# Performance work log

Hardware: AMD Instinct MI355X
Metric: run time of the kernel (lower is better)

Reference implementation:

```python
import jax, jax.numpy as jnp
import numpy as np

N_NODES = 30000
N_EDGES = 480000
F_IN = 64
F_EDGE = 16
HID = 128
N_LAYERS = 3
N_CLASSES = 10
MSG_EPS = 1e-7   # GENConv eps added after ReLU
SM_EPS = 1e-16   # PyG softmax denom eps
LN_EPS = 1e-5


def _layer_norm(x, g, b):
    m = jnp.mean(x, axis=-1, keepdims=True)
    v = jnp.mean((x - m) ** 2, axis=-1, keepdims=True)
    return (x - m) * jax.lax.rsqrt(v + LN_EPS) * g + b


def _gen_conv(h, ea, src, dst, t, w1, b1, lg, lb, w2, b2):
    # GENConv message: relu(x_j + e_ij) + eps  -> [E, H]
    msg = jax.nn.relu(h[src] + ea) + MSG_EPS
    # learnable-temperature segment softmax over incoming edges of each node
    logits = msg * t
    mx = jax.ops.segment_max(logits, dst, num_segments=N_NODES)
    e = jnp.exp(logits - mx[dst])
    s = jax.ops.segment_sum(e, dst, num_segments=N_NODES)
    alpha = e / (s[dst] + SM_EPS)
    agg = jax.ops.segment_sum(msg * alpha, dst, num_segments=N_NODES)  # [N, H]
    # out = MLP(aggr + x): Linear(H,2H) -> LayerNorm -> ReLU -> Linear(2H,H)
    z = agg + h
    z = jax.nn.relu(_layer_norm(z @ w1 + b1, lg, lb)) @ w2 + b2
    return z


def setup_inputs() -> dict:
    key = jax.random.key(0)
    ks = jax.random.split(key, 10)
    g = lambda k, s, sc=0.05: jax.random.normal(k, s, jnp.float32) * sc
    return {
        "x": g(ks[0], (N_NODES, F_IN), 1.0),
        "edge_attr": g(ks[1], (N_EDGES, F_EDGE), 1.0),
        "node_enc_w": g(ks[2], (F_IN, HID)),
        "node_enc_b": jnp.zeros((HID,), jnp.float32),
        "edge_enc_w": g(ks[3], (F_EDGE, HID)),
        "edge_enc_b": jnp.zeros((HID,), jnp.float32),
        "mlp1_w": g(ks[4], (N_LAYERS, HID, 2 * HID)),
        "mlp1_b": jnp.zeros((N_LAYERS, 2 * HID), jnp.float32),
        "mlp_ln_g": jnp.ones((N_LAYERS, 2 * HID), jnp.float32),
        "mlp_ln_b": jnp.zeros((N_LAYERS, 2 * HID), jnp.float32),
        "mlp2_w": g(ks[5], (N_LAYERS, 2 * HID, HID)),
        "mlp2_b": jnp.zeros((N_LAYERS, HID), jnp.float32),
        "t": jnp.ones((N_LAYERS,), jnp.float32),
        "norm_g": jnp.ones((N_LAYERS, HID), jnp.float32),
        "norm_b": jnp.zeros((N_LAYERS, HID), jnp.float32),
        "lin_w": g(ks[6], (HID, N_CLASSES)),
        "lin_b": jnp.zeros((N_CLASSES,), jnp.float32),
        "edge_index": jax.random.randint(ks[7], (2, N_EDGES), 0, N_NODES, jnp.int32),
    }


def reference(x, edge_attr, node_enc_w, node_enc_b, edge_enc_w, edge_enc_b,
              mlp1_w, mlp1_b, mlp_ln_g, mlp_ln_b, mlp2_w, mlp2_b, t,
              norm_g, norm_b, lin_w, lin_b, edge_index):
    src, dst = edge_index[0], edge_index[1]
    ea = edge_attr @ edge_enc_w + edge_enc_b   # [E, H]
    h = x @ node_enc_w + node_enc_b            # [N, H]
    # first layer applies the conv directly (as in the original forward)
    h = _gen_conv(h, ea, src, dst, t[0], mlp1_w[0], mlp1_b[0],
                  mlp_ln_g[0], mlp_ln_b[0], mlp2_w[0], mlp2_b[0])
    # remaining DeepGCN res+ layers: h = h + conv(dropout(relu(norm(h))))
    for i in range(1, N_LAYERS):
        res = h
        z = jax.nn.relu(_layer_norm(h, norm_g[i], norm_b[i]))  # dropout p=0.1 -> identity in eval
        z = _gen_conv(z, ea, src, dst, t[i], mlp1_w[i], mlp1_b[i],
                      mlp_ln_g[i], mlp_ln_b[i], mlp2_w[i], mlp2_b[i])
        h = z + res
    # final norm/act from layers[0] then classifier (dropout -> identity in eval)
    h = jax.nn.relu(_layer_norm(h, norm_g[0], norm_b[0]))
    return h @ lin_w + lin_b
```

## Files before the change

### kernel.cpp

```cpp
#include <hip/hip_runtime.h>
#include <hip/hip_bf16.h>

#define NN 30000
#define NE 480000
#define NROWT 1875

typedef __attribute__((ext_vector_type(8))) short short8;
typedef __attribute__((ext_vector_type(4))) float floatx4;

__device__ __forceinline__ short f2bs(float f) {
    __hip_bfloat16 h = __float2bfloat16(f);
    return *reinterpret_cast<short*>(&h);
}

__device__ __forceinline__ short2 split_bf16(float f) {
    __hip_bfloat16 h = __float2bfloat16(f);
    float r = f - __bfloat162float(h);
    __hip_bfloat16 l = __float2bfloat16(r);
    short2 out;
    out.x = *reinterpret_cast<short*>(&h);
    out.y = *reinterpret_cast<short*>(&l);
    return out;
}

__global__ void presplit_all(const float* __restrict__ ew, const float* __restrict__ nw,
                             const float* __restrict__ m1w, const float* __restrict__ m2w,
                             const float* __restrict__ lw,
                             short* __restrict__ ew_h, short* __restrict__ ew_l,
                             short* __restrict__ nw_h, short* __restrict__ nw_l,
                             short* __restrict__ m1_h, short* __restrict__ m1_l,
                             short* __restrict__ m2_h, short* __restrict__ m2_l,
                             short* __restrict__ lw_h, short* __restrict__ lw_l)
{
    int i = blockIdx.x * 256 + threadIdx.x;
    if (i < 2048) {
        int k = i >> 7, n = i & 127;
        short2 s = split_bf16(ew[i]);
        ew_h[n * 16 + k] = s.x; ew_l[n * 16 + k] = s.y;
    } else if (i < 10240) {
        int j = i - 2048;
        int k = j >> 7, n = j & 127;
        short2 s = split_bf16(nw[j]);
        nw_h[n * 64 + k] = s.x; nw_l[n * 64 + k] = s.y;
    } else if (i < 108544) {
        int j = i - 10240;
        int l = j >> 15, jj = j & 32767;
        int k = jj >> 8, n = jj & 255;
        short2 s = split_bf16(m1w[j]);
        m1_h[(size_t)l * 32768 + n * 128 + k] = s.x;
        m1_l[(size_t)l * 32768 + n * 128 + k] = s.y;
    } else if (i < 206848) {
        int j = i - 108544;
        int l = j >> 15, jj = j & 32767;
        int k = jj >> 7, n = jj & 127;
        short2 s = split_bf16(m2w[j]);
        m2_h[(size_t)l * 32768 + n * 256 + k] = s.x;
        m2_l[(size_t)l * 32768 + n * 256 + k] = s.y;
    } else if (i < 208896) {
        int j = i - 206848;
        int k = j >> 4, n = j & 15;
        short2 s = (n < 10) ? split_bf16(lw[k * 10 + n]) : short2{0, 0};
        lw_h[n * 128 + k] = s.x; lw_l[n * 128 + k] = s.y;
    }
}

template<int K, int N>
__launch_bounds__(256)
__global__ void gemm_a32(const float* __restrict__ A, const short* __restrict__ Bh,
                         const short* __restrict__ Bl, const float* __restrict__ bias,
                         float* __restrict__ C, unsigned* __restrict__ hp, int total_waves)
{
    int wave = ((blockIdx.x * 256) + threadIdx.x) >> 6;
    if (wave >= total_waves) return;
    constexpr int NT = N / 16;
    const int mt = wave / NT, nt = wave % NT;
    const int lane = threadIdx.x & 63;
    const int l15 = lane & 15, quad = lane >> 4;
    const int row = mt * 16 + l15;
    const int col = nt * 16 + l15;
    floatx4 acc = {0.f, 0.f, 0.f, 0.f};
#pragma unroll
    for (int k0 = 0; k0 < K; k0 += 32) {
        const int kb = k0 + quad * 8;
        short8 ah, al;
        const float* ap = A + (size_t)row * K + kb;
        floatx4 a0 = *(const floatx4*)ap;
        floatx4 a1 = *(const floatx4*)(ap + 4);
#pragma unroll
        for (int j = 0; j < 4; j++) {
            short2 s0 = split_bf16(a0[j]); ah[j] = s0.x; al[j] = s0.y;
            short2 s1 = split_bf16(a1[j]); ah[j + 4] = s1.x; al[j + 4] = s1.y;
        }
        short8 bh = *(const short8*)(Bh + (size_t)col * K + kb);
        short8 bl = *(const short8*)(Bl + (size_t)col * K + kb);
        acc = __builtin_amdgcn_mfma_f32_16x16x32_bf16(ah, bh, acc, 0, 0, 0);
        acc = __builtin_amdgcn_mfma_f32_16x16x32_bf16(al, bh, acc, 0, 0, 0);
        acc = __builtin_amdgcn_mfma_f32_16x16x32_bf16(ah, bl, acc, 0, 0, 0);
    }
    float bv = bias[col];
#pragma unroll
    for (int r = 0; r < 4; r++) {
        int ro = mt * 16 + quad * 4 + r;
        float v = acc[r] + bv;
        C[(size_t)ro * N + col] = v;
        int mb = (int)(unsigned short)f2bs(v);
        int ob = __shfl_xor(mb, 1, 64);
        if ((l15 & 1) == 0)
            hp[(size_t)ro * 64 + nt * 8 + (l15 >> 1)] = (unsigned)mb | ((unsigned)ob << 16);
    }
}

template<int K, int NTOT, int NTW, int NREAL>
__launch_bounds__(256)
__global__ void gemm_s(const short* __restrict__ Ah, const short* __restrict__ Al,
                       const short* __restrict__ Bh, const short* __restrict__ Bl,
                       const float* __restrict__ bias, float* __restrict__ C, int total_waves)
{
    int wave = ((blockIdx.x * 256) + threadIdx.x) >> 6;
    if (wave >= total_waves) return;
    constexpr int NG = NTOT / (16 * NTW);
    const int mt = wave / NG, g = wave % NG;
    const int lane = threadIdx.x & 63;
    const int l15 = lane & 15, quad = lane >> 4;
    const int row = mt * 16 + l15;
    floatx4 acc[NTW];
#pragma unroll
    for (int t = 0; t < NTW; t++) acc[t] = {0.f, 0.f, 0.f, 0.f};
#pragma unroll
    for (int k0 = 0; k0 < K; k0 += 32) {
        const int kb = k0 + quad * 8;
        short8 ah = *(const short8*)(Ah + (size_t)row * K + kb);
        short8 al = *(const short8*)(Al + (size_t)row * K + kb);
#pragma unroll
        for (int t = 0; t < NTW; t++) {
            int col = g * NTW * 16 + t * 16 + l15;
            short8 bh = *(const short8*)(Bh + (size_t)col * K + kb);
            short8 bl = *(const short8*)(Bl + (size_t)col * K + kb);
            acc[t] = __builtin_amdgcn_mfma_f32_16x16x32_bf16(ah, bh, acc[t], 0, 0, 0);
            acc[t] = __builtin_amdgcn_mfma_f32_16x16x32_bf16(al, bh, acc[t], 0, 0, 0);
            acc[t] = __builtin_amdgcn_mfma_f32_16x16x32_bf16(ah, bl, acc[t], 0, 0, 0);
        }
    }
#pragma unroll
    for (int t = 0; t < NTW; t++) {
        int col = g * NTW * 16 + t * 16 + l15;
        if (col < NREAL) {
            float bv = bias[col];
#pragma unroll
            for (int r = 0; r < 4; r++) {
                int ro = mt * 16 + quad * 4 + r;
                C[(size_t)ro * NREAL + col] = acc[t][r] + bv;
            }
        }
    }
}

__launch_bounds__(256)
__global__ void gemm_ea(const float* __restrict__ edge_attr, const int* __restrict__ eidx_csr,
                        const short* __restrict__ Bh, const short* __restrict__ Bl,
                        const float* __restrict__ bias, unsigned* __restrict__ ea4)
{
    __shared__ short tile[2][16][132];
    const int wv = threadIdx.x >> 6;
    const int sub = wv >> 1, g = wv & 1;
    const int lane = threadIdx.x & 63;
    const int l15 = lane & 15, quad = lane >> 4;
    const int p = blockIdx.x * 32 + sub * 16 + l15;
    short8 a;
    if (quad < 2) {
        int e = eidx_csr[p];
        const float* ap = edge_attr + (size_t)e * 16 + quad * 8;
        floatx4 a0 = *(const floatx4*)ap;
        floatx4 a1 = *(const floatx4*)(ap + 4);
#pragma unroll
        for (int j = 0; j < 4; j++) { a[j] = f2bs(a0[j]); a[j + 4] = f2bs(a1[j]); }
    } else {
#pragma unroll
        for (int j = 0; j < 8; j++) a[j] = 0;
    }
    floatx4 acc[4];
#pragma unroll
    for (int t = 0; t < 4; t++) acc[t] = {0.f, 0.f, 0.f, 0.f};
#pragma unroll
    for (int t = 0; t < 4; t++) {
        int col = g * 64 + t * 16 + l15;
        short8 bh, bl;
        if (quad < 2) {
            bh = *(const short8*)(Bh + (size_t)col * 16 + quad * 8);
            bl = *(const short8*)(Bl + (size_t)col * 16 + quad * 8);
        } else {
#pragma unroll
            for (int j = 0; j < 8; j++) { bh[j] = 0; bl[j] = 0; }
        }
        acc[t] = __builtin_amdgcn_mfma_f32_16x16x32_bf16(a, bh, acc[t], 0, 0, 0);
        acc[t] = __builtin_amdgcn_mfma_f32_16x16x32_bf16(a, bl, acc[t], 0, 0, 0);
    }
#pragma unroll
    for (int t = 0; t < 4; t++) {
        int col = g * 64 + t * 16 + l15;
        float bv = bias[col];
#pragma unroll
        for (int r = 0; r < 4; r++)
            tile[sub][quad * 4 + r][col] = f2bs(acc[t][r] + bv);
    }
    __syncthreads();
#pragma unroll
    for (int c = 0; c < 2; c++) {
        int idx = threadIdx.x + 256 * c;
        int o = idx * 16;
        int g4l = o >> 10;
        int lp = (o & 1023) >> 4;
        unsigned u[4];
#pragma unroll
        for (int e = 0; e < 4; e++) {
            int rl = g4l * 4 + e;
            u[e] = *(const unsigned*)&tile[rl >> 4][rl & 15][2 * lp];
        }
        uint4 val = make_uint4(u[0], u[1], u[2], u[3]);
        *(uint4*)((char*)ea4 + (size_t)blockIdx.x * 8192 + o) = val;
    }
}

__global__ void zero_kernel(int* __restrict__ p, int n)
{
    int i = blockIdx.x * 256 + threadIdx.x;
    if (i < n) p[i] = 0;
}

__global__ void hist_kernel(const int* __restrict__ dst, int* __restrict__ count)
{
    int e = blockIdx.x * 256 + threadIdx.x;
    if (e < NE) atomicAdd(count + dst[e], 1);
}

__launch_bounds__(1024)
__global__ void scan_kernel(const int* __restrict__ count, int* __restrict__ rowptr)
{
    __shared__ int part[1024];
    const int t = threadIdx.x;
    const int CH = (NN + 1023) / 1024;
    const int base = t * CH;
    int sum = 0;
    for (int j = 0; j < CH; j++) {
        int idx = base + j;
        if (idx < NN) sum += count[idx];
    }
    part[t] = sum;
    __syncthreads();
    for (int d = 1; d < 1024; d <<= 1) {
        int v = (t >= d) ? part[t - d] : 0;
        __syncthreads();
        part[t] += v;
        __syncthreads();
    }
    int off = (t == 0) ? 0 : part[t - 1];
    for (int j = 0; j < CH; j++) {
        int idx = base + j;
        if (idx < NN) { rowptr[idx] = off; off += count[idx]; }
    }
    if (t == 1023) rowptr[NN] = part[1023];
}

__global__ void scatter_kernel(const int* __restrict__ src, const int* __restrict__ dst,
                               const int* __restrict__ rowptr, int* __restrict__ cursor,
                               int* __restrict__ src_csr, int* __restrict__ eidx_csr)
{
    int e = blockIdx.x * 256 + threadIdx.x;
    if (e >= NE) return;
    int d = dst[e];
    int pos = rowptr[d] + atomicAdd(cursor + d, 1);
    src_csr[pos] = src[e];
    eidx_csr[pos] = e;
}

__device__ __forceinline__ void updm(float hv, float av, float tt, float m,
                                     float& s, float& n)
{
    float g = fmaxf(hv + av, 0.f) + 1e-7f;
    float e = __expf(g * tt) * m;
    s += e;
    n = fmaf(g, e, n);
}

__launch_bounds__(256)
__global__ void agg_kernel(const unsigned* __restrict__ hp, const float* __restrict__ hres,
                           const uint4* __restrict__ ea4q, const int* __restrict__ src_csr,
                           const int* __restrict__ rowptr, const float* __restrict__ tptr,
                           int layer, short* __restrict__ Zh, short* __restrict__ Zl)
{
    int node = (blockIdx.x * 256 + threadIdx.x) >> 6;
    if (node >= NN) return;
    const int lane = threadIdx.x & 63;
    const float tt = tptr[layer];
    const int start = rowptr[node];
    const int end = rowptr[node + 1];
    const int g0 = start >> 2, g1 = (end + 3) >> 2;
    float s0 = 0.f, s1 = 0.f, n0 = 0.f, n1 = 0.f;
    float s0b = 0.f, s1b = 0.f, n0b = 0.f, n1b = 0.f;

#define PROC(GG, S0, S1, N0, N1)                                                   \
    {                                                                              \
        uint4 uu = ea4q[((size_t)(GG) << 6) + lane];                               \
        int4 sv = *(const int4*)(src_csr + 4 * (GG));                              \
        int jb = 4 * (GG);                                                         \
        float m0 = (jb     >= start && jb     < end) ? 1.f : 0.f;                  \
        float m1 = (jb + 1 >= start && jb + 1 < end) ? 1.f : 0.f;                  \
        float m2 = (jb + 2 >= start && jb + 2 < end) ? 1.f : 0.f;                  \
        float m3 = (jb + 3 >= start && jb + 3 < end) ? 1.f : 0.f;                  \
        unsigned ha = hp[(size_t)sv.x * 64 + lane];                                \
        unsigned hb = hp[(size_t)sv.y * 64 + lane];                                \
        unsigned hc = hp[(size_t)sv.z * 64 + lane];                                \
        unsigned hd = hp[(size_t)sv.w * 64 + lane];                                \
        updm(__uint_as_float(ha << 16), __uint_as_float(uu.x << 16), tt, m0, S0, N0); \
        updm(__uint_as_float(ha & 0xffff0000u), __uint_as_float(uu.x & 0xffff0000u), tt, m0, S1, N1); \
        updm(__uint_as_float(hb << 16), __uint_as_float(uu.y << 16), tt, m1, S0, N0); \
        updm(__uint_as_float(hb & 0xffff0000u), __uint_as_float(uu.y & 0xffff0000u), tt, m1, S1, N1); \
        updm(__uint_as_float(hc << 16), __uint_as_float(uu.z << 16), tt, m2, S0, N0); \
        updm(__uint_as_float(hc & 0xffff0000u), __uint_as_float(uu.z & 0xffff0000u), tt, m2, S1, N1); \
        updm(__uint_as_float(hd << 16), __uint_as_float(uu.w << 16), tt, m3, S0, N0); \
        updm(__uint_as_float(hd & 0xffff0000u), __uint_as_float(uu.w & 0xffff0000u), tt, m3, S1, N1); \
    }

    int g = g0;
    for (; g + 2 <= g1; g += 2) {
        PROC(g, s0, s1, n0, n1);
        PROC(g + 1, s0b, s1b, n0b, n1b);
    }
    if (g < g1) PROC(g, s0, s1, n0, n1);
#undef PROC
    s0 += s0b; s1 += s1b; n0 += n0b; n1 += n1b;

    float2 res = ((const float2*)hres)[(size_t)node * 64 + lane];
    float ox = n0 / (s0 + 1e-16f) + res.x;
    float oy = n1 / (s1 + 1e-16f) + res.y;
    short2 sx = split_bf16(ox), sy = split_bf16(oy);
    ((unsigned*)Zh)[(size_t)node * 64 + lane] =
        (unsigned)(unsigned short)sx.x | ((unsigned)(unsigned short)sy.x << 16);
    ((unsigned*)Zl)[(size_t)node * 64 + lane] =
        (unsigned)(unsigned short)sx.y | ((unsigned)(unsigned short)sy.y << 16);
}

template<bool HAS_RES, bool FINAL>
__launch_bounds__(256)
__global__ void mlp_fused(const short* __restrict__ Ah, const short* __restrict__ Al,
                          const short* __restrict__ B1h, const short* __restrict__ B1l,
                          const float* __restrict__ b1, const float* __restrict__ g1,
                          const float* __restrict__ be1,
                          const short* __restrict__ B2h, const short* __restrict__ B2l,
                          const float* __restrict__ b2, const float* __restrict__ res,
                          const float* __restrict__ g2, const float* __restrict__ be2,
                          short* __restrict__ z1h,
                          float* __restrict__ Hout, float* __restrict__ HinOut,
                          unsigned* __restrict__ HP,
                          short* __restrict__ Fh, short* __restrict__ Fl)
{
    __shared__ __align__(16) short lds[32768];
    const int wv = threadIdx.x >> 6;
    const int lane = threadIdx.x & 63;
    const int l15 = lane & 15, quad = lane >> 4;
    const int tile = blockIdx.x * 4 + wv;
    const bool valid = (tile < NROWT);
    const int row = tile * 16 + l15;

    floatx4 acc[16];
#pragma unroll
    for (int t = 0; t < 16; t++) acc[t] = {0.f, 0.f, 0.f, 0.f};
    for (int hf = 0; hf < 2; hf++) {
        __syncthreads();
        {
            const float4* s1p = (const float4*)(B1h + hf * 16384);
            const float4* s2p = (const float4*)(B1l + hf * 16384);
            float4* d = (float4*)lds;
#pragma unroll
            for (int i = 0; i < 8; i++) {
                int t8 = threadIdx.x + 256 * i;
                int col = t8 >> 4, k8 = t8 & 15;
                int unit = col * 16 + (k8 ^ (col & 15));
                d[unit] = s1p[t8];
                d[2048 + unit] = s2p[t8];
            }
        }
        __syncthreads();
        if (valid) {
#pragma unroll
            for (int k0 = 0; k0 < 128; k0 += 32) {
                const int kb = k0 + quad * 8;
                const int kb8 = kb >> 3;
                short8 ah = *(const short8*)(Ah + (size_t)row * 128 + kb);
                short8 al = *(const short8*)(Al + (size_t)row * 128 + kb);
#pragma unroll
                for (int t = 0; t < 8; t++) {
                    int col = t * 16 + l15;
                    int unit = col * 16 + (kb8 ^ (col & 15));
                    const short* bp = lds + unit * 8;
                    short8 bh = *(const short8*)bp;
                    short8 bl = *(const short8*)(bp + 16384);
                    int ti = hf * 8 + t;
                    acc[ti] = __builtin_amdgcn_mfma_f32_16x16x32_bf16(ah, bh, acc[ti], 0, 0, 0);
                    acc[ti] = __builtin_amdgcn_mfma_f32_16x16x32_bf16(al, bh, acc[ti], 0, 0, 0);
                    acc[ti] = __builtin_amdgcn_mfma_f32_16x16x32_bf16(ah, bl, acc[ti], 0, 0, 0);
                }
            }
        }
    }
    if (valid) {
#pragma unroll
        for (int t = 0; t < 16; t++) {
            float bv = b1[t * 16 + l15];
#pragma unroll
            for (int r = 0; r < 4; r++) acc[t][r] += bv;
        }
        float s1[4] = {0.f, 0.f, 0.f, 0.f}, s2[4] = {0.f, 0.f, 0.f, 0.f};
#pragma unroll
        for (int t = 0; t < 16; t++)
#pragma unroll
            for (int r = 0; r < 4; r++) { s1[r] += acc[t][r]; s2[r] += acc[t][r] * acc[t][r]; }
#pragma unroll
        for (int m = 1; m <= 8; m <<= 1)
#pragma unroll
            for (int r = 0; r < 4; r++) {
                s1[r] += __shfl_xor(s1[r], m, 64);
                s2[r] += __shfl_xor(s2[r], m, 64);
            }
        float mean[4], rstd[4];
#pragma unroll
        for (int r = 0; r < 4; r++) {
            mean[r] = s1[r] * (1.f / 256.f);
            float var = s2[r] * (1.f / 256.f) - mean[r] * mean[r];
            rstd[r] = rsqrtf(var + 1e-5f);
        }
#pragma unroll
        for (int t = 0; t < 16; t++) {
            int col = t * 16 + l15;
            float gg = g1[col], bb = be1[col];
#pragma unroll
            for (int r = 0; r < 4; r++) {
                float y = fmaxf((acc[t][r] - mean[r]) * rstd[r] * gg + bb, 0.f);
                int ro = tile * 16 + quad * 4 + r;
                z1h[(size_t)ro * 256 + col] = f2bs(y);
            }
        }
    }
    floatx4 acc2[8];
#pragma unroll
    for (int t = 0; t < 8; t++) acc2[t] = {0.f, 0.f, 0.f, 0.f};
    for (int hf = 0; hf < 2; hf++) {
        __syncthreads();
        {
            const float4* s1p = (const float4*)(B2h + hf * 16384);
            const float4* s2p = (const float4*)(B2l + hf * 16384);
            float4* d = (float4*)lds;
#pragma unroll
            for (int i = 0; i < 8; i++) {
                int t8 = threadIdx.x + 256 * i;
                int col = t8 >> 5, k8 = t8 & 31;
                int unit = col * 32 + (k8 ^ (col & 15));
                d[unit] = s1p[t8];
                d[2048 + unit] = s2p[t8];
            }
        }
        __syncthreads();
        if (valid) {
#pragma unroll
            for (int k0 = 0; k0 < 256; k0 += 32) {
                const int kb = k0 + quad * 8;
                const int kb8 = kb >> 3;
                short8 zh = *(const short8*)(z1h + (size_t)row * 256 + kb);
#pragma unroll
                for (int t = 0; t < 4; t++) {
                    int col = t * 16 + l15;
                    int unit = col * 32 + (kb8 ^ (col & 15));
                    const short* bp = lds + unit * 8;
                    short8 bh = *(const short8*)bp;
                    short8 bl = *(const short8*)(bp + 16384);
                    int ti = hf * 4 + t;
                    acc2[ti] = __builtin_amdgcn_mfma_f32_16x16x32_bf16(zh, bh, acc2[ti], 0, 0, 0);
                    acc2[ti] = __builtin_amdgcn_mfma_f32_16x16x32_bf16(zh, bl, acc2[ti], 0, 0, 0);
                }
            }
        }
    }
    if (valid) {
#pragma unroll
        for (int t = 0; t < 8; t++) {
            int col = t * 16 + l15;
            float bv = b2[col];
#pragma unroll
            for (int r = 0; r < 4; r++) {
                acc2[t][r] += bv;
                if (HAS_RES) {
                    int ro = tile * 16 + quad * 4 + r;
                    acc2[t][r] += res[(size_t)ro * 128 + col];
                }
            }
        }
        float s1[4] = {0.f, 0.f, 0.f, 0.f}, s2[4] = {0.f, 0.f, 0.f, 0.f};
#pragma unroll
        for (int t = 0; t < 8; t++)
#pragma unroll
            for (int r = 0; r < 4; r++) { s1[r] += acc2[t][r]; s2[r] += acc2[t][r] * acc2[t][r]; }
#pragma unroll
        for (int m = 1; m <= 8; m <<= 1)
#pragma unroll
            for (int r = 0; r < 4; r++) {
                s1[r] += __shfl_xor(s1[r], m, 64);
                s2[r] += __shfl_xor(s2[r], m, 64);
            }
        float mean[4], rstd[4];
#pragma unroll
        for (int r = 0; r < 4; r++) {
            mean[r] = s1[r] * (1.f / 128.f);
            float var = s2[r] * (1.f / 128.f) - mean[r] * mean[r];
            rstd[r] = rsqrtf(var + 1e-5f);
        }
#pragma unroll
        for (int t = 0; t < 8; t++) {
            int col = t * 16 + l15;
            float gg = g2[col], bb = be2[col];
#pragma unroll
            for (int r = 0; r < 4; r++) {
                int ro = tile * 16 + quad * 4 + r;
                float x = acc2[t][r];
                float y = fmaxf((x - mean[r]) * rstd[r] * gg + bb, 0.f);
                if (FINAL) {
                    short2 sp = split_bf16(y);
                    Fh[(size_t)ro * 128 + col] = sp.x;
                    Fl[(size_t)ro * 128 + col] = sp.y;
                } else {
                    Hout[(size_t)ro * 128 + col] = x;
                    HinOut[(size_t)ro * 128 + col] = y;
                    int yb = (int)(unsigned short)f2bs(y);
                    int ob = __shfl_xor(yb, 1, 64);
                    if ((l15 & 1) == 0)
                        HP[(size_t)ro * 64 + t * 8 + (l15 >> 1)] =
                            (unsigned)yb | ((unsigned)ob << 16);
                }
            }
        }
    }
}

extern "C" void kernel_launch(void* const* d_in, const int* in_sizes, int n_in,
                              void* d_out, int out_size, void* d_ws, size_t ws_size,
                              hipStream_t stream)
{
    const float* x         = (const float*)d_in[0];
    const float* edge_attr = (const float*)d_in[1];
    const float* nw        = (const float*)d_in[2];
    const float* nb        = (const float*)d_in[3];
    const float* ew        = (const float*)d_in[4];
    const float* eb        = (const float*)d_in[5];
    const float* m1w       = (const float*)d_in[6];
    const float* m1b       = (const float*)d_in[7];
    const float* lng       = (const float*)d_in[8];
    const float* lnb       = (const float*)d_in[9];
    const float* m2w       = (const float*)d_in[10];
    const float* m2b       = (const float*)d_in[11];
    const float* tpr       = (const float*)d_in[12];
    const float* ng        = (const float*)d_in[13];
    const float* nbb       = (const float*)d_in[14];
    const float* lw        = (const float*)d_in[15];
    const float* lb        = (const float*)d_in[16];
    const int* ei  = (const int*)d_in[17];
    const int* src = ei;
    const int* dst = ei + NE;

    char* w = (char*)d_ws;
    unsigned* ea4 = (unsigned*)w; w += (size_t)NE * 128 * 2;
    int* src_csr  = (int*)w; w += (size_t)NE * 4;
    int* eidx_csr = (int*)w; w += (size_t)NE * 4;
    unsigned* hp  = (unsigned*)w; w += (size_t)NN * 64 * 4;
    float* h   = (float*)w; w += (size_t)NN * 128 * 4;
    float* hin = (float*)w; w += (size_t)NN * 128 * 4;
    short* zbuf_h = (short*)w; w += (size_t)NN * 128 * 2;
    short* zbuf_l = (short*)w; w += (size_t)NN * 128 * 2;
    short* fin_h  = (short*)w; w += (size_t)NN * 128 * 2;
    short* fin_l  = (short*)w; w += (size_t)NN * 128 * 2;
    short* z1s_h  = (short*)w; w += (size_t)NN * 256 * 2;
    short* ew_h = (short*)w; w += (size_t)128 * 16 * 2;
    short* ew_l = (short*)w; w += (size_t)128 * 16 * 2;
    short* nw_h = (short*)w; w += (size_t)128 * 64 * 2;
    short* nw_l = (short*)w; w += (size_t)128 * 64 * 2;
    short* m1_h = (short*)w; w += (size_t)3 * 256 * 128 * 2;
    short* m1_l = (short*)w; w += (size_t)3 * 256 * 128 * 2;
    short* m2_h = (short*)w; w += (size_t)3 * 128 * 256 * 2;
    short* m2_l = (short*)w; w += (size_t)3 * 128 * 256 * 2;
    short* lw_h = (short*)w; w += (size_t)16 * 128 * 2;
    short* lw_l = (short*)w; w += (size_t)16 * 128 * 2;
    int* count  = (int*)w;   w += (size_t)NN * 4;
    int* cursor = (int*)w;   w += (size_t)NN * 4;
    int* rowptr = (int*)w;   w += (size_t)(NN + 1) * 4;

    zero_kernel<<<(2 * NN + 255) / 256, 256, 0, stream>>>(count, 2 * NN);
    hist_kernel<<<(NE + 255) / 256, 256, 0, stream>>>(dst, count);
    scan_kernel<<<1, 1024, 0, stream>>>(count, rowptr);
    scatter_kernel<<<(NE + 255) / 256, 256, 0, stream>>>(src, dst, rowptr, cursor,
                                                         src_csr, eidx_csr);

    presplit_all<<<(208896 + 255) / 256, 256, 0, stream>>>(
        ew, nw, m1w, m2w, lw, ew_h, ew_l, nw_h, nw_l, m1_h, m1_l, m2_h, m2_l, lw_h, lw_l);

    gemm_ea<<<NE / 32, 256, 0, stream>>>(edge_attr, eidx_csr, ew_h, ew_l, eb, ea4);
    gemm_a32<64, 128><<<(NN / 16) * 8 / 4, 256, 0, stream>>>(x, nw_h, nw_l, nb, h, hp,
                                                             (NN / 16) * 8);

    const uint4* ea4q = (const uint4*)ea4;
    const int mgrid = (NROWT + 3) / 4;
    for (int layer = 0; layer < 3; ++layer) {
        const float* hi = (layer == 0) ? h : hin;
        agg_kernel<<<NN / 4, 256, 0, stream>>>(hp, hi, ea4q, src_csr, rowptr, tpr, layer,
                                               zbuf_h, zbuf_l);
        if (layer == 0) {
            mlp_fused<false, false><<<mgrid, 256, 0, stream>>>(
                zbuf_h, zbuf_l, m1_h, m1_l, m1b, lng, lnb,
                m2_h, m2_l, m2b, nullptr, ng + 128, nbb + 128,
                z1s_h, h, hin, hp, nullptr, nullptr);
        } else if (layer == 1) {
            mlp_fused<true, false><<<mgrid, 256, 0, stream>>>(
                zbuf_h, zbuf_l, m1_h + 32768, m1_l + 32768, m1b + 256, lng + 256, lnb + 256,
                m2_h + 32768, m2_l + 32768, m2b + 128, h, ng + 256, nbb + 256,
                z1s_h, h, hin, hp, nullptr, nullptr);
        } else {
            mlp_fused<true, true><<<mgrid, 256, 0, stream>>>(
                zbuf_h, zbuf_l, m1_h + 65536, m1_l + 65536, m1b + 512, lng + 512, lnb + 512,
                m2_h + 65536, m2_l + 65536, m2b + 256, h, ng, nbb,
                z1s_h, nullptr, nullptr, nullptr, fin_h, fin_l);
        }
    }
    gemm_s<128, 16, 1, 10><<<((NN / 16) + 3) / 4, 256, 0, stream>>>(
        fin_h, fin_l, lw_h, lw_l, lb, (float*)d_out, NN / 16);
}
```

Baseline: 484.3 us.

## Drop low bf16 split for aggregated input and unroll edge loop four ways

The aggregation kernel now writes one bf16 copy of its output instead of a hi/lo split pair, and the first MLP GEMM drops the matching lo*hi MFMA. This halves that intermediate's write and read traffic and removes a third of the MFMAs in the first GEMM. The edge loop is also unrolled four ways with separate accumulators to expose more memory-level parallelism on the gathers. Accuracy of the MLP input drops to plain bf16, which could exceed tolerance.

```diff
diff --git a/kernel.cpp b/kernel.cpp
--- a/kernel.cpp
+++ b/kernel.cpp
@@ -286,7 +286,7 @@
 __global__ void agg_kernel(const unsigned* __restrict__ hp, const float* __restrict__ hres,
                            const uint4* __restrict__ ea4q, const int* __restrict__ src_csr,
                            const int* __restrict__ rowptr, const float* __restrict__ tptr,
-                           int layer, short* __restrict__ Zh, short* __restrict__ Zl)
+                           int layer, unsigned* __restrict__ Zp)
 {
     int node = (blockIdx.x * 256 + threadIdx.x) >> 6;
     if (node >= NN) return;
@@ -295,10 +295,10 @@
     const int start = rowptr[node];
     const int end = rowptr[node + 1];
     const int g0 = start >> 2, g1 = (end + 3) >> 2;
-    float s0 = 0.f, s1 = 0.f, n0 = 0.f, n1 = 0.f;
-    float s0b = 0.f, s1b = 0.f, n0b = 0.f, n1b = 0.f;
-
-#define PROC(GG, S0, S1, N0, N1)                                                   \
+    float S0[4] = {0.f, 0.f, 0.f, 0.f}, S1[4] = {0.f, 0.f, 0.f, 0.f};
+    float N0[4] = {0.f, 0.f, 0.f, 0.f}, N1[4] = {0.f, 0.f, 0.f, 0.f};
+
+#define PROC(GG, U)                                                                \
     {                                                                              \
         uint4 uu = ea4q[((size_t)(GG) << 6) + lane];                               \
         int4 sv = *(const int4*)(src_csr + 4 * (GG));                              \
@@ -311,38 +311,40 @@
         unsigned hb = hp[(size_t)sv.y * 64 + lane];                                \
         unsigned hc = hp[(size_t)sv.z * 64 + lane];                                \
         unsigned hd = hp[(size_t)sv.w * 64 + lane];                                \
-        updm(__uint_as_float(ha << 16), __uint_as_float(uu.x << 16), tt, m0, S0, N0); \
-        updm(__uint_as_float(ha & 0xffff0000u), __uint_as_float(uu.x & 0xffff0000u), tt, m0, S1, N1); \
-        updm(__uint_as_float(hb << 16), __uint_as_float(uu.y << 16), tt, m1, S0, N0); \
-        updm(__uint_as_float(hb & 0xffff0000u), __uint_as_float(uu.y & 0xffff0000u), tt, m1, S1, N1); \
-        updm(__uint_as_float(hc << 16), __uint_as_float(uu.z << 16), tt, m2, S0, N0); \
-        updm(__uint_as_float(hc & 0xffff0000u), __uint_as_float(uu.z & 0xffff0000u), tt, m2, S1, N1); \
-        updm(__uint_as_float(hd << 16), __uint_as_float(uu.w << 16), tt, m3, S0, N0); \
-        updm(__uint_as_float(hd & 0xffff0000u), __uint_as_float(uu.w & 0xffff0000u), tt, m3, S1, N1); \
+        updm(__uint_as_float(ha << 16), __uint_as_float(uu.x << 16), tt, m0, S0[U], N0[U]); \
+        updm(__uint_as_float(ha & 0xffff0000u), __uint_as_float(uu.x & 0xffff0000u), tt, m0, S1[U], N1[U]); \
+        updm(__uint_as_float(hb << 16), __uint_as_float(uu.y << 16), tt, m1, S0[U], N0[U]); \
+        updm(__uint_as_float(hb & 0xffff0000u), __uint_as_float(uu.y & 0xffff0000u), tt, m1, S1[U], N1[U]); \
+        updm(__uint_as_float(hc << 16), __uint_as_float(uu.z << 16), tt, m2, S0[U], N0[U]); \
+        updm(__uint_as_float(hc & 0xffff0000u), __uint_as_float(uu.z & 0xffff0000u), tt, m2, S1[U], N1[U]); \
+        updm(__uint_as_float(hd << 16), __uint_as_float(uu.w << 16), tt, m3, S0[U], N0[U]); \
+        updm(__uint_as_float(hd & 0xffff0000u), __uint_as_float(uu.w & 0xffff0000u), tt, m3, S1[U], N1[U]); \
     }
 
     int g = g0;
-    for (; g + 2 <= g1; g += 2) {
-        PROC(g, s0, s1, n0, n1);
-        PROC(g + 1, s0b, s1b, n0b, n1b);
-    }
-    if (g < g1) PROC(g, s0, s1, n0, n1);
+    for (; g + 4 <= g1; g += 4) {
+        PROC(g,     0);
+        PROC(g + 1, 1);
+        PROC(g + 2, 2);
+        PROC(g + 3, 3);
+    }
+    for (; g < g1; g++) PROC(g, 0);
 #undef PROC
-    s0 += s0b; s1 += s1b; n0 += n0b; n1 += n1b;
+    float s0 = (S0[0] + S0[1]) + (S0[2] + S0[3]);
+    float s1 = (S1[0] + S1[1]) + (S1[2] + S1[3]);
+    float n0 = (N0[0] + N0[1]) + (N0[2] + N0[3]);
+    float n1 = (N1[0] + N1[1]) + (N1[2] + N1[3]);
 
     float2 res = ((const float2*)hres)[(size_t)node * 64 + lane];
     float ox = n0 / (s0 + 1e-16f) + res.x;
     float oy = n1 / (s1 + 1e-16f) + res.y;
-    short2 sx = split_bf16(ox), sy = split_bf16(oy);
-    ((unsigned*)Zh)[(size_t)node * 64 + lane] =
-        (unsigned)(unsigned short)sx.x | ((unsigned)(unsigned short)sy.x << 16);
-    ((unsigned*)Zl)[(size_t)node * 64 + lane] =
-        (unsigned)(unsigned short)sx.y | ((unsigned)(unsigned short)sy.y << 16);
+    Zp[(size_t)node * 64 + lane] =
+        (unsigned)(unsigned short)f2bs(ox) | ((unsigned)(unsigned short)f2bs(oy) << 16);
 }
 
 template<bool HAS_RES, bool FINAL>
 __launch_bounds__(256)
-__global__ void mlp_fused(const short* __restrict__ Ah, const short* __restrict__ Al,
+__global__ void mlp_fused(const short* __restrict__ Ap,
                           const short* __restrict__ B1h, const short* __restrict__ B1l,
                           const float* __restrict__ b1, const float* __restrict__ g1,
                           const float* __restrict__ be1,
@@ -386,8 +388,7 @@
             for (int k0 = 0; k0 < 128; k0 += 32) {
                 const int kb = k0 + quad * 8;
                 const int kb8 = kb >> 3;
-                short8 ah = *(const short8*)(Ah + (size_t)row * 128 + kb);
-                short8 al = *(const short8*)(Al + (size_t)row * 128 + kb);
+                short8 ah = *(const short8*)(Ap + (size_t)row * 128 + kb);
 #pragma unroll
                 for (int t = 0; t < 8; t++) {
                     int col = t * 16 + l15;
@@ -397,7 +398,6 @@
                     short8 bl = *(const short8*)(bp + 16384);
                     int ti = hf * 8 + t;
                     acc[ti] = __builtin_amdgcn_mfma_f32_16x16x32_bf16(ah, bh, acc[ti], 0, 0, 0);
-                    acc[ti] = __builtin_amdgcn_mfma_f32_16x16x32_bf16(al, bh, acc[ti], 0, 0, 0);
                     acc[ti] = __builtin_amdgcn_mfma_f32_16x16x32_bf16(ah, bl, acc[ti], 0, 0, 0);
                 }
             }
@@ -570,10 +570,9 @@
     int* src_csr  = (int*)w; w += (size_t)NE * 4;
     int* eidx_csr = (int*)w; w += (size_t)NE * 4;
     unsigned* hp  = (unsigned*)w; w += (size_t)NN * 64 * 4;
+    unsigned* zp  = (unsigned*)w; w += (size_t)NN * 64 * 4;
     float* h   = (float*)w; w += (size_t)NN * 128 * 4;
     float* hin = (float*)w; w += (size_t)NN * 128 * 4;
-    short* zbuf_h = (short*)w; w += (size_t)NN * 128 * 2;
-    short* zbuf_l = (short*)w; w += (size_t)NN * 128 * 2;
     short* fin_h  = (short*)w; w += (size_t)NN * 128 * 2;
     short* fin_l  = (short*)w; w += (size_t)NN * 128 * 2;
     short* z1s_h  = (short*)w; w += (size_t)NN * 256 * 2;
@@ -608,21 +607,20 @@
     const int mgrid = (NROWT + 3) / 4;
     for (int layer = 0; layer < 3; ++layer) {
         const float* hi = (layer == 0) ? h : hin;
-        agg_kernel<<<NN / 4, 256, 0, stream>>>(hp, hi, ea4q, src_csr, rowptr, tpr, layer,
-                                               zbuf_h, zbuf_l);
+        agg_kernel<<<NN / 4, 256, 0, stream>>>(hp, hi, ea4q, src_csr, rowptr, tpr, layer, zp);
         if (layer == 0) {
             mlp_fused<false, false><<<mgrid, 256, 0, stream>>>(
-                zbuf_h, zbuf_l, m1_h, m1_l, m1b, lng, lnb,
+                (const short*)zp, m1_h, m1_l, m1b, lng, lnb,
                 m2_h, m2_l, m2b, nullptr, ng + 128, nbb + 128,
                 z1s_h, h, hin, hp, nullptr, nullptr);
         } else if (layer == 1) {
             mlp_fused<true, false><<<mgrid, 256, 0, stream>>>(
-                zbuf_h, zbuf_l, m1_h + 32768, m1_l + 32768, m1b + 256, lng + 256, lnb + 256,
+                (const short*)zp, m1_h + 32768, m1_l + 32768, m1b + 256, lng + 256, lnb + 256,
                 m2_h + 32768, m2_l + 32768, m2b + 128, h, ng + 256, nbb + 256,
                 z1s_h, h, hin, hp, nullptr, nullptr);
         } else {
             mlp_fused<true, true><<<mgrid, 256, 0, stream>>>(
-                zbuf_h, zbuf_l, m1_h + 65536, m1_l + 65536, m1b + 512, lng + 512, lnb + 512,
+                (const short*)zp, m1_h + 65536, m1_l + 65536, m1b + 512, lng + 512, lnb + 512,
                 m2_h + 65536, m2_l + 65536, m2b + 256, h, ng, nbb,
                 z1s_h, nullptr, nullptr, nullptr, fin_h, fin_l);
         }
```

Result: no change. 487.9 us (+0.7%).
